# Optimization experiments

Hardware: AMD Instinct MI355X
Metric: run time of the kernel (lower is better)

Reference implementation:

```python
import jax, jax.numpy as jnp
import numpy as np

B, L, D = 1, 512, 1280


def setup_inputs() -> dict:
    key = jax.random.key(0)
    k1, k2, k3 = jax.random.split(key, 3)
    prev_result = jax.random.normal(k1, (B, L, D), dtype=jnp.float32)
    # nn.Linear(2*D, 2): store weight as [2D, 2] so forward is x @ W + b
    W = jax.random.normal(k2, (2 * D, 2), dtype=jnp.float32) * (1.0 / np.sqrt(2 * D))
    b = jax.random.normal(k3, (2,), dtype=jnp.float32) * 0.01
    return {"prev_result": prev_result, "W": W, "b": b}


def reference(prev_result, W, b):
    # Dropout is identity at inference. The torch code builds
    # pairwise = cat(x_i * x_j, x_i - x_j) of shape [B,L,L,2D] then applies
    # Linear(2D, 2). We fuse: split W into the prod half Wp and diff half Wd.
    Wp, Wd = W[:D], W[D:]                                   # each [D, 2]
    # (x_i * x_j) @ Wp  -- bilinear contraction, no [B,L,L,2D] intermediate
    prod_term = jnp.einsum('bid,bjd,dk->bijk', prev_result, prev_result, Wp)
    # (x_i - x_j) @ Wd = (x @ Wd)_i - (x @ Wd)_j
    d_proj = prev_result @ Wd                                # [B, L, 2]
    diff_term = d_proj[:, :, None, :] - d_proj[:, None, :, :]
    prediction = prod_term + diff_term + b                   # [B, L, L, 2]
    prediction = (prediction + prediction.transpose(0, 2, 1, 3)) / 2
    return prediction[:, 1:-1, 1:-1]                         # [B, L-2, L-2, 2]
```

## Files before the change

### kernel.cpp

```cpp
#include <hip/hip_runtime.h>
#include <math.h>

#define D_DIM 1280
#define ODIM  510
#define KSTEPS 40
#define QK    320

typedef short bf16x8 __attribute__((ext_vector_type(8)));
typedef float f32x4  __attribute__((ext_vector_type(4)));

__device__ __forceinline__ unsigned pkbf(float a, float b) {
  unsigned ua = __float_as_uint(a), ub = __float_as_uint(b);
  return ((ua + 0x8000u) >> 16) | ((ub + 0x8000u) & 0xffff0000u);
}

__global__ __launch_bounds__(256, 1) void pcmd_prep(
    const float* __restrict__ X,
    const float* __restrict__ W,
    unsigned short* __restrict__ Xbf,
    unsigned short* __restrict__ A0,
    unsigned short* __restrict__ A1)
{
  __shared__ unsigned short sG[3][10][64][8];

  const int R   = (int)blockIdx.x >> 2;
  const int q   = (int)blockIdx.x & 3;
  const int tid = threadIdx.x;

  for (int task = tid; task < 640; task += 256) {
    const int lr = task / 40;
    const int gc = task - lr * 40;
    const int s = gc >> 2, quad = gc & 3;
    const int prow = R * 16 + lr;
    uint4 vx = {0,0,0,0}, v0 = {0,0,0,0}, v1 = {0,0,0,0};
    if (prow <= 510) {
      const float* px = X + (size_t)(prow + 1) * D_DIM + q * QK + gc * 8;
      float4 x0 = *(const float4*)px;
      float4 x1 = *(const float4*)(px + 4);
      const float* pw = W + 2 * (q * QK + gc * 8);
      float4 w0 = *(const float4*)(pw +  0);
      float4 w1 = *(const float4*)(pw +  4);
      float4 w2 = *(const float4*)(pw +  8);
      float4 w3 = *(const float4*)(pw + 12);
      vx.x = pkbf(x0.x, x0.y);            vx.y = pkbf(x0.z, x0.w);
      vx.z = pkbf(x1.x, x1.y);            vx.w = pkbf(x1.z, x1.w);
      v0.x = pkbf(x0.x*w0.x, x0.y*w0.z);  v0.y = pkbf(x0.z*w1.x, x0.w*w1.z);
      v0.z = pkbf(x1.x*w2.x, x1.y*w2.z);  v0.w = pkbf(x1.z*w3.x, x1.w*w3.z);
      v1.x = pkbf(x0.x*w0.y, x0.y*w0.w);  v1.y = pkbf(x0.z*w1.y, x0.w*w1.w);
      v1.z = pkbf(x1.x*w2.y, x1.y*w2.w);  v1.w = pkbf(x1.z*w3.y, x1.w*w3.w);
    }
    const int swzl = quad * 16 + ((lr + quad + 4 * s) & 15);
    *(uint4*)&sG[0][s][swzl][0] = vx;
    *(uint4*)&sG[1][s][swzl][0] = v0;
    *(uint4*)&sG[2][s][swzl][0] = v1;
  }
  __syncthreads();

  for (int g = tid; g < 640; g += 256) {
    const int s = g >> 6, l = g & 63;
    const int quad = l >> 4, m = l & 15;
    const int swzl = quad * 16 + ((m + quad + 4 * s) & 15);
    const size_t go = ((size_t)((R * KSTEPS + q * 10 + s) * 64) + l) * 8;
    *(uint4*)(Xbf + go) = *(const uint4*)&sG[0][s][swzl][0];
    *(uint4*)(A0  + go) = *(const uint4*)&sG[1][s][swzl][0];
    *(uint4*)(A1  + go) = *(const uint4*)&sG[2][s][swzl][0];
  }
}

__global__ __launch_bounds__(256, 2) void pcmd_gemm(
    const unsigned short* __restrict__ Xbf,
    const unsigned short* __restrict__ A0,
    const unsigned short* __restrict__ A1,
    const float* __restrict__ b,
    float* __restrict__ out)
{
  __shared__ float sR[4][2][16][17];

  const int t = (int)blockIdx.x;
  int bi = (int)((65.0 - sqrt(4225.0 - 8.0 * (double)t)) * 0.5);
  {
    int s0 = bi * 32 - (bi * (bi - 1)) / 2;
    if (t < s0) { --bi; }
    int s1 = (bi + 1) * 32 - ((bi + 1) * bi) / 2;
    if (t >= s1) { ++bi; }
  }
  const int start = bi * 32 - (bi * (bi - 1)) / 2;
  const int bj = bi + (t - start);

  const int tid  = threadIdx.x;
  const int lane = tid & 63;
  const int wv   = tid >> 6;

  const unsigned short* pa0 = A0  + ((size_t)(bi * KSTEPS + wv * 10) * 64 + lane) * 8;
  const unsigned short* pa1 = A1  + ((size_t)(bi * KSTEPS + wv * 10) * 64 + lane) * 8;
  const unsigned short* pb  = Xbf + ((size_t)(bj * KSTEPS + wv * 10) * 64 + lane) * 8;

  bf16x8 ra0[4], ra1[4], rb[4];
  #pragma unroll
  for (int s = 0; s < 4; ++s) {
    ra0[s] = *(const bf16x8*)(pa0 + s * 512);
    ra1[s] = *(const bf16x8*)(pa1 + s * 512);
    rb[s]  = *(const bf16x8*)(pb  + s * 512);
  }

  f32x4 acc0 = {0.f, 0.f, 0.f, 0.f};
  f32x4 acc1 = {0.f, 0.f, 0.f, 0.f};

  #pragma unroll
  for (int s = 0; s < 10; ++s) {
    const int cur = s & 3;
    bf16x8 a0 = ra0[cur], a1 = ra1[cur], bb = rb[cur];
    if (s + 4 < 10) {
      ra0[cur] = *(const bf16x8*)(pa0 + (s + 4) * 512);
      ra1[cur] = *(const bf16x8*)(pa1 + (s + 4) * 512);
      rb[cur]  = *(const bf16x8*)(pb  + (s + 4) * 512);
    }
    acc0 = __builtin_amdgcn_mfma_f32_16x16x32_bf16(a0, bb, acc0, 0, 0, 0);
    acc1 = __builtin_amdgcn_mfma_f32_16x16x32_bf16(a1, bb, acc1, 0, 0, 0);
  }

  const int m = lane & 15, quad = lane >> 4;
  #pragma unroll
  for (int r = 0; r < 4; ++r) {
    sR[wv][0][quad * 4 + r][m] = acc0[r];
    sR[wv][1][quad * 4 + r][m] = acc1[r];
  }
  __syncthreads();

  const float b0 = b[0], b1 = b[1];
  const int il = tid >> 4, jl = tid & 15;

  {
    const int oi = bi * 16 + il, oj = bj * 16 + jl;
    if (oi < ODIM && oj < ODIM) {
      float2 v;
      v.x = sR[0][0][il][jl] + sR[1][0][il][jl] + sR[2][0][il][jl] + sR[3][0][il][jl] + b0;
      v.y = sR[0][1][il][jl] + sR[1][1][il][jl] + sR[2][1][il][jl] + sR[3][1][il][jl] + b1;
      *(float2*)(out + ((size_t)oi * ODIM + oj) * 2) = v;
    }
  }
  if (bi != bj) {
    const int oi = bj * 16 + il, oj = bi * 16 + jl;
    if (oi < ODIM && oj < ODIM) {
      float2 v;
      v.x = sR[0][0][jl][il] + sR[1][0][jl][il] + sR[2][0][jl][il] + sR[3][0][jl][il] + b0;
      v.y = sR[0][1][jl][il] + sR[1][1][jl][il] + sR[2][1][jl][il] + sR[3][1][jl][il] + b1;
      *(float2*)(out + ((size_t)oi * ODIM + oj) * 2) = v;
    }
  }
}

extern "C" void kernel_launch(void* const* d_in, const int* in_sizes, int n_in,
                              void* d_out, int out_size, void* d_ws, size_t ws_size,
                              hipStream_t stream) {
  const float* X = (const float*)d_in[0];
  const float* W = (const float*)d_in[1];
  const float* b = (const float*)d_in[2];
  float* out = (float*)d_out;
  (void)in_sizes; (void)n_in; (void)out_size; (void)ws_size;

  const size_t PLANE = (size_t)512 * D_DIM;
  unsigned short* Xbf = (unsigned short*)d_ws;
  unsigned short* A0  = Xbf + PLANE;
  unsigned short* A1  = A0 + PLANE;

  hipLaunchKernelGGL(pcmd_prep, dim3(128), dim3(256), 0, stream, X, W, Xbf, A0, A1);
  hipLaunchKernelGGL(pcmd_gemm, dim3(528), dim3(256), 0, stream, Xbf, A0, A1, b, out);
}
```

Measured before the change: 70.15 us.

## Split GEMM K-reduction across eight waves per block instead of four

Doubles the gemm block to 512 threads so each of eight waves handles five K-steps instead of ten, loading all operands up front and dropping the rotating prefetch. The cross-wave reduction in shared memory grows to eight partials, and the two output writes (direct and transposed) are split between the two thread halves instead of run in sequence. The aim is more memory-level parallelism and shorter per-wave dependency chains in this latency-bound kernel, at the cost of more shared memory, more reduction work and a larger block per CU.

Measured after the change: 70.69 us. About the same (+0.8%).

```diff
diff --git a/kernel.cpp b/kernel.cpp
--- a/kernel.cpp
+++ b/kernel.cpp
@@ -67,14 +67,14 @@
   }
 }
 
-__global__ __launch_bounds__(256, 2) void pcmd_gemm(
+__global__ __launch_bounds__(512, 4) void pcmd_gemm(
     const unsigned short* __restrict__ Xbf,
     const unsigned short* __restrict__ A0,
     const unsigned short* __restrict__ A1,
     const float* __restrict__ b,
     float* __restrict__ out)
 {
-  __shared__ float sR[4][2][16][17];
+  __shared__ float sR[8][2][16][17];
 
   const int t = (int)blockIdx.x;
   int bi = (int)((65.0 - sqrt(4225.0 - 8.0 * (double)t)) * 0.5);
@@ -91,13 +91,13 @@
   const int lane = tid & 63;
   const int wv   = tid >> 6;
 
-  const unsigned short* pa0 = A0  + ((size_t)(bi * KSTEPS + wv * 10) * 64 + lane) * 8;
-  const unsigned short* pa1 = A1  + ((size_t)(bi * KSTEPS + wv * 10) * 64 + lane) * 8;
-  const unsigned short* pb  = Xbf + ((size_t)(bj * KSTEPS + wv * 10) * 64 + lane) * 8;
+  const unsigned short* pa0 = A0  + ((size_t)(bi * KSTEPS + wv * 5) * 64 + lane) * 8;
+  const unsigned short* pa1 = A1  + ((size_t)(bi * KSTEPS + wv * 5) * 64 + lane) * 8;
+  const unsigned short* pb  = Xbf + ((size_t)(bj * KSTEPS + wv * 5) * 64 + lane) * 8;
 
-  bf16x8 ra0[4], ra1[4], rb[4];
+  bf16x8 ra0[5], ra1[5], rb[5];
   #pragma unroll
-  for (int s = 0; s < 4; ++s) {
+  for (int s = 0; s < 5; ++s) {
     ra0[s] = *(const bf16x8*)(pa0 + s * 512);
     ra1[s] = *(const bf16x8*)(pa1 + s * 512);
     rb[s]  = *(const bf16x8*)(pb  + s * 512);
@@ -105,18 +105,10 @@
 
   f32x4 acc0 = {0.f, 0.f, 0.f, 0.f};
   f32x4 acc1 = {0.f, 0.f, 0.f, 0.f};
-
   #pragma unroll
-  for (int s = 0; s < 10; ++s) {
-    const int cur = s & 3;
-    bf16x8 a0 = ra0[cur], a1 = ra1[cur], bb = rb[cur];
-    if (s + 4 < 10) {
-      ra0[cur] = *(const bf16x8*)(pa0 + (s + 4) * 512);
-      ra1[cur] = *(const bf16x8*)(pa1 + (s + 4) * 512);
-      rb[cur]  = *(const bf16x8*)(pb  + (s + 4) * 512);
-    }
-    acc0 = __builtin_amdgcn_mfma_f32_16x16x32_bf16(a0, bb, acc0, 0, 0, 0);
-    acc1 = __builtin_amdgcn_mfma_f32_16x16x32_bf16(a1, bb, acc1, 0, 0, 0);
+  for (int s = 0; s < 5; ++s) {
+    acc0 = __builtin_amdgcn_mfma_f32_16x16x32_bf16(ra0[s], rb[s], acc0, 0, 0, 0);
+    acc1 = __builtin_amdgcn_mfma_f32_16x16x32_bf16(ra1[s], rb[s], acc1, 0, 0, 0);
   }
 
   const int m = lane & 15, quad = lane >> 4;
@@ -128,23 +120,24 @@
   __syncthreads();
 
   const float b0 = b[0], b1 = b[1];
-  const int il = tid >> 4, jl = tid & 15;
 
-  {
+  if (tid < 256) {
+    const int il = tid >> 4, jl = tid & 15;
     const int oi = bi * 16 + il, oj = bj * 16 + jl;
     if (oi < ODIM && oj < ODIM) {
-      float2 v;
-      v.x = sR[0][0][il][jl] + sR[1][0][il][jl] + sR[2][0][il][jl] + sR[3][0][il][jl] + b0;
-      v.y = sR[0][1][il][jl] + sR[1][1][il][jl] + sR[2][1][il][jl] + sR[3][1][il][jl] + b1;
+      float2 v; v.x = b0; v.y = b1;
+      #pragma unroll
+      for (int w = 0; w < 8; ++w) { v.x += sR[w][0][il][jl]; v.y += sR[w][1][il][jl]; }
       *(float2*)(out + ((size_t)oi * ODIM + oj) * 2) = v;
     }
-  }
-  if (bi != bj) {
+  } else if (bi != bj) {
+    const int tt = tid - 256;
+    const int il = tt >> 4, jl = tt & 15;
     const int oi = bj * 16 + il, oj = bi * 16 + jl;
     if (oi < ODIM && oj < ODIM) {
-      float2 v;
-      v.x = sR[0][0][jl][il] + sR[1][0][jl][il] + sR[2][0][jl][il] + sR[3][0][jl][il] + b0;
-      v.y = sR[0][1][jl][il] + sR[1][1][jl][il] + sR[2][1][jl][il] + sR[3][1][jl][il] + b1;
+      float2 v; v.x = b0; v.y = b1;
+      #pragma unroll
+      for (int w = 0; w < 8; ++w) { v.x += sR[w][0][jl][il]; v.y += sR[w][1][jl][il]; }
       *(float2*)(out + ((size_t)oi * ODIM + oj) * 2) = v;
     }
   }
@@ -165,5 +158,5 @@
   unsigned short* A1  = A0 + PLANE;
 
   hipLaunchKernelGGL(pcmd_prep, dim3(128), dim3(256), 0, stream, X, W, Xbf, A0, A1);
-  hipLaunchKernelGGL(pcmd_gemm, dim3(528), dim3(256), 0, stream, Xbf, A0, A1, b, out);
+  hipLaunchKernelGGL(pcmd_gemm, dim3(528), dim3(512), 0, stream, Xbf, A0, A1, b, out);
 }
```
